# Kernel optimization log

Measured on AMD Instinct MI355X. Metric: run time of the kernel, lower is better.

## Reference

```python
import jax, jax.numpy as jnp
import numpy as np

N, B, S, F_DIM, E = 100000, 4096, 32, 256, 256


def _linear_params(key, fan_in, fan_out):
    kw, kb = jax.random.split(key)
    bound = 1.0 / np.sqrt(fan_in)
    W = jax.random.uniform(kw, (fan_in, fan_out), jnp.float32, -bound, bound)
    b = jax.random.uniform(kb, (fan_out,), jnp.float32, -bound, bound)
    return W, b


def setup_inputs() -> dict:
    key = jax.random.key(0)
    ks = jax.random.split(key, 10)
    Wm, bm = _linear_params(ks[4], F_DIM, E)
    Wq, bq = _linear_params(ks[5], F_DIM, E)
    Wk, bk = _linear_params(ks[6], F_DIM, E)
    Wv, bv = _linear_params(ks[7], F_DIM, E)
    Wc, bc = _linear_params(ks[8], 2 * E, E)
    return {
        "nodes": jax.random.randint(ks[0], (B,), 0, N),
        "neigh_mean": jax.random.randint(ks[1], (B, S), 0, N),
        "neigh_attn": jax.random.randint(ks[2], (B, S), 0, N),
        "id2feat": jax.random.normal(ks[3], (N, F_DIM), jnp.float32),
        "Wm": Wm, "bm": bm,
        "Wq": Wq, "bq": bq,
        "Wk": Wk, "bk": bk,
        "Wv": Wv, "bv": bv,
        "Wc": Wc, "bc": bc,
    }


def reference(nodes, neigh_mean, neigh_attn, id2feat,
              Wm, bm, Wq, bq, Wk, bk, Wv, bv, Wc, bc):
    self_feats = id2feat[nodes]                                   # [B, F]

    # MeanAggregator1: per-row mean of W(id2feat[neighbors]).
    # (mean(W x + b) == W mean(x) + b by linearity; all rows have S neighbors)
    ctx = jnp.mean(id2feat[neigh_mean], axis=1) @ Wm + bm          # [B, E]

    # AttnAggregator1: self-query attention over [neighbors ; self].
    neigh = id2feat[neigh_attn]                                    # [B, S, F]
    cat = jnp.concatenate([neigh, self_feats[:, None, :]], axis=1)  # [B, S+1, F]
    Q = self_feats @ Wq + bq                                       # [B, E]
    K = cat @ Wk + bk                                              # [B, S+1, E]
    V = cat @ Wv + bv                                              # [B, S+1, E]
    scores = jnp.einsum('be,bse->bs', Q, K)                        # [B, S+1]
    # Torch mask loop with uniform neighbor length S masks column S (the self slot)
    pad_mask = jnp.arange(S + 1) >= S                              # [S+1]
    scores = jnp.where(pad_mask[None, :], -jnp.inf, scores)
    attn = jax.nn.softmax(scores, axis=-1)
    mix = jnp.einsum('bs,bse->be', attn, V)                        # [B, E]

    combined = jnp.tanh(jnp.concatenate([mix, ctx], axis=-1) @ Wc + bc)  # [B, E]
    norm = jnp.linalg.norm(combined, axis=-1, keepdims=True)
    return combined / jnp.maximum(norm, 1e-12)                     # F.normalize(p=2)
```

## Files before the change

kernel.cpp:

```cpp
#include <hip/hip_runtime.h>
#include <math.h>

#define S_NEI 32

__global__ __launch_bounds__(256) void transpose256(const float* __restrict__ in,
                                                    float* __restrict__ outT) {
    __shared__ float tile[32][33];
    const int bx = blockIdx.x * 32, by = blockIdx.y * 32;
    const int x = threadIdx.x, y = threadIdx.y;
#pragma unroll
    for (int i = 0; i < 32; i += 8)
        tile[y + i][x] = in[(by + y + i) * 256 + bx + x];
    __syncthreads();
#pragma unroll
    for (int i = 0; i < 32; i += 8)
        outT[(bx + y + i) * 256 + by + x] = tile[x][y + i];
}

template <int KT>
__device__ __forceinline__ void gemm_tile8(const float* __restrict__ A, int row0,
                                           const float* __restrict__ B,
                                           float acc[2][4], float* __restrict__ sA,
                                           float* __restrict__ sB) {
    const int t = threadIdx.x;
    const int tr = t >> 6, tc = t & 63;
    const int r = t >> 5;
    const int k1 = t & 31;
    const size_t arow = (size_t)(row0 + r) * KT;
    for (int kb = 0; kb < KT; kb += 32) {
        sA[k1 * 12 + r] = A[arow + kb + k1];
#pragma unroll
        for (int i = 0; i < 8; ++i) {
            *reinterpret_cast<float4*>(&sB[(i * 4 + tr) * 256 + tc * 4]) =
                *reinterpret_cast<const float4*>(&B[(size_t)(kb + i * 4 + tr) * 256 + tc * 4]);
        }
        __syncthreads();
#pragma unroll
        for (int k = 0; k < 32; ++k) {
            const float2 a2 = *reinterpret_cast<const float2*>(&sA[k * 12 + tr * 2]);
            const float4 b4 = *reinterpret_cast<const float4*>(&sB[k * 256 + tc * 4]);
            acc[0][0] += a2.x * b4.x; acc[0][1] += a2.x * b4.y;
            acc[0][2] += a2.x * b4.z; acc[0][3] += a2.x * b4.w;
            acc[1][0] += a2.y * b4.x; acc[1][1] += a2.y * b4.y;
            acc[1][2] += a2.y * b4.z; acc[1][3] += a2.y * b4.w;
        }
        __syncthreads();
    }
}

__global__ __launch_bounds__(256) void precompute3(const float* __restrict__ Wq,
                                                   const float* __restrict__ Wv,
                                                   const float* __restrict__ Wm,
                                                   const float* __restrict__ Wc,
                                                   const float* __restrict__ WkT,
                                                   float* __restrict__ Wqk,
                                                   float* __restrict__ Wvc,
                                                   float* __restrict__ Wmc) {
    __shared__ float sA[32 * 12];
    __shared__ float sB[32 * 256];
    float acc[2][4] = {};
    const float *Ap, *Bp;
    float* Cp;
    switch (blockIdx.y) {
        case 0: Ap = Wq; Bp = WkT; Cp = Wqk; break;
        case 1: Ap = Wv; Bp = Wc; Cp = Wvc; break;
        default: Ap = Wm; Bp = Wc + 256 * 256; Cp = Wmc; break;
    }
    const int row0 = blockIdx.x * 8;
    gemm_tile8<256>(Ap, row0, Bp, acc, sA, sB);
    const int tr = threadIdx.x >> 6, tc = threadIdx.x & 63;
#pragma unroll
    for (int i = 0; i < 2; ++i) {
        float4 v = make_float4(acc[i][0], acc[i][1], acc[i][2], acc[i][3]);
        *reinterpret_cast<float4*>(&Cp[(row0 + tr * 2 + i) * 256 + tc * 4]) = v;
    }
}

__global__ __launch_bounds__(256) void bias_k(const float* __restrict__ bq,
                                              const float* __restrict__ bv,
                                              const float* __restrict__ bm,
                                              const float* __restrict__ bc,
                                              const float* __restrict__ Wc,
                                              const float* __restrict__ WkT,
                                              float* __restrict__ bqk,
                                              float* __restrict__ bfull) {
    const int c = blockIdx.x;
    const int e = threadIdx.x;
    const int w = e >> 6, l = e & 63;
    float a = bq[e] * WkT[e * 256 + c];
    float v = bv[e] * Wc[e * 256 + c] + bm[e] * Wc[(256 + e) * 256 + c];
    __shared__ float redA[4], redV[4];
#pragma unroll
    for (int off = 32; off; off >>= 1) { a += __shfl_xor(a, off); v += __shfl_xor(v, off); }
    if (l == 0) { redA[w] = a; redV[w] = v; }
    __syncthreads();
    if (e == 0) {
        bqk[c] = redA[0] + redA[1] + redA[2] + redA[3];
        bfull[c] = bc[c] + redV[0] + redV[1] + redV[2] + redV[3];
    }
}


#define SAF4(k) ((k) * 4 + ((((k) >> 3)) << 2))

#define FMA44(a4, b4)                                                       \
    do {                                                                    \
        acc[0][0] += (a4).x * (b4).x; acc[0][1] += (a4).x * (b4).y;         \
        acc[0][2] += (a4).x * (b4).z; acc[0][3] += (a4).x * (b4).w;         \
        acc[1][0] += (a4).y * (b4).x; acc[1][1] += (a4).y * (b4).y;         \
        acc[1][2] += (a4).y * (b4).z; acc[1][3] += (a4).y * (b4).w;         \
        acc[2][0] += (a4).z * (b4).x; acc[2][1] += (a4).z * (b4).y;         \
        acc[2][2] += (a4).z * (b4).z; acc[2][3] += (a4).z * (b4).w;         \
        acc[3][0] += (a4).w * (b4).x; acc[3][1] += (a4).w * (b4).y;         \
        acc[3][2] += (a4).w * (b4).z; acc[3][3] += (a4).w * (b4).w;         \
    } while (0)

__global__ __launch_bounds__(256, 2) void fused4(const float* __restrict__ id2feat,
                                                 const int* __restrict__ nodes,
                                                 const int* __restrict__ neigh_mean,
                                                 const int* __restrict__ neigh_attn,
                                                 const float* __restrict__ Wqk,
                                                 const float* __restrict__ bqk,
                                                 const float* __restrict__ Wfused,
                                                 const float* __restrict__ bfull,
                                                 float* __restrict__ out) {
    __shared__ __align__(16) char smem[18112];
    float* R0  = (float*)smem;
    float* sQk = (float*)(smem + 12480);
    int*   sIA = (int*)(smem + 16640);
    int*   sIM = (int*)(smem + 17152);

    const int t = threadIdx.x;
    const int w = t >> 6, l = t & 63;
    const int kq = w;
    const int col4 = l * 4;
    const int row0 = blockIdx.x * 4;

    if (t < 128) sIA[t] = neigh_attn[(size_t)row0 * S_NEI + t];
    else sIM[t - 128] = neigh_mean[(size_t)row0 * S_NEI + (t - 128)];

    {
        const float4 v = *reinterpret_cast<const float4*>(
            &id2feat[(size_t)nodes[row0 + w] * 256 + col4]);
        R0[SAF4(col4 + 0) + w] = v.x;
        R0[SAF4(col4 + 1) + w] = v.y;
        R0[SAF4(col4 + 2) + w] = v.z;
        R0[SAF4(col4 + 3) + w] = v.w;
    }
    __syncthreads();

    float acc[4][4] = {};

    {
        const float* Bp = Wqk + (size_t)(kq * 64) * 256 + col4;
        float4 bufA[8], bufB[8];
#pragma unroll
        for (int j = 0; j < 8; ++j)
            bufA[j] = *reinterpret_cast<const float4*>(&Bp[(size_t)j * 256]);
        for (int kb = 0; kb < 64; kb += 16) {
#pragma unroll
            for (int j = 0; j < 8; ++j)
                bufB[j] = *reinterpret_cast<const float4*>(&Bp[(size_t)(kb + 8 + j) * 256]);
#pragma unroll
            for (int j = 0; j < 8; ++j) {
                const float4 a4 = *reinterpret_cast<const float4*>(&R0[SAF4(kq * 64 + kb + j)]);
                FMA44(a4, bufA[j]);
            }
            if (kb + 16 < 64) {
#pragma unroll
                for (int j = 0; j < 8; ++j)
                    bufA[j] = *reinterpret_cast<const float4*>(&Bp[(size_t)(kb + 16 + j) * 256]);
            }
#pragma unroll
            for (int j = 0; j < 8; ++j) {
                const float4 a4 =
                    *reinterpret_cast<const float4*>(&R0[SAF4(kq * 64 + kb + 8 + j)]);
                FMA44(a4, bufB[j]);
            }
        }
    }
    __syncthreads();
    if (kq) {
        float* p = R0 + ((kq - 1) * 4) * 260 + col4;
#pragma unroll
        for (int r = 0; r < 4; ++r) {
            p[r * 260 + 0] = acc[r][0]; p[r * 260 + 1] = acc[r][1];
            p[r * 260 + 2] = acc[r][2]; p[r * 260 + 3] = acc[r][3];
        }
    }
    __syncthreads();
    if (kq == 0) {
        const float4 bq4 = *reinterpret_cast<const float4*>(&bqk[col4]);
#pragma unroll
        for (int r = 0; r < 4; ++r) {
            float v0 = acc[r][0] + bq4.x, v1 = acc[r][1] + bq4.y;
            float v2 = acc[r][2] + bq4.z, v3 = acc[r][3] + bq4.w;
#pragma unroll
            for (int s = 0; s < 3; ++s) {
                const float* p = R0 + (s * 4 + r) * 260 + col4;
                v0 += p[0]; v1 += p[1]; v2 += p[2]; v3 += p[3];
            }
            sQk[r * 260 + col4 + 0] = v0; sQk[r * 260 + col4 + 1] = v1;
            sQk[r * 260 + col4 + 2] = v2; sQk[r * 260 + col4 + 3] = v3;
        }
    }
    __syncthreads();

    {
        const int b = w;
        const float4 q = *reinterpret_cast<const float4*>(&sQk[b * 260 + col4]);
        const float4* f4 = reinterpret_cast<const float4*>(id2feat);
        const int* ia = sIA + b * 32;
        const int* im = sIM + b * 32;
        float4 macc = make_float4(0.f, 0.f, 0.f, 0.f);
        float4 wa = make_float4(0.f, 0.f, 0.f, 0.f);
        float m = -1e30f, e = 0.f;
#pragma unroll
        for (int cch = 0; cch < 4; ++cch) {
            float4 r[8];
#pragma unroll
            for (int j = 0; j < 8; ++j) r[j] = f4[(size_t)ia[cch * 8 + j] * 64 + l];
#pragma unroll
            for (int j = 0; j < 8; ++j) {
                const float4 v = f4[(size_t)im[cch * 8 + j] * 64 + l];
                macc.x += v.x; macc.y += v.y; macc.z += v.z; macc.w += v.w;
            }
            float p[8];
#pragma unroll
            for (int j = 0; j < 8; ++j) {
                float s = q.x * r[j].x + q.y * r[j].y + q.z * r[j].z + q.w * r[j].w;
#pragma unroll
                for (int off = 32; off; off >>= 1) s += __shfl_xor(s, off);
                p[j] = s;
            }
            float cm = p[0];
#pragma unroll
            for (int j = 1; j < 8; ++j) cm = fmaxf(cm, p[j]);
            const float newm = fmaxf(m, cm);
            const float sc = __expf(m - newm);
            e *= sc; wa.x *= sc; wa.y *= sc; wa.z *= sc; wa.w *= sc;
#pragma unroll
            for (int j = 0; j < 8; ++j) {
                const float g = __expf(p[j] - newm);
                e += g;
                wa.x += g * r[j].x; wa.y += g * r[j].y;
                wa.z += g * r[j].z; wa.w += g * r[j].w;
            }
            m = newm;
        }
        const float inv = 1.0f / e;
        const float mix[4] = {wa.x * inv, wa.y * inv, wa.z * inv, wa.w * inv};
        const float mev[4] = {macc.x * (1.f / 32), macc.y * (1.f / 32),
                              macc.z * (1.f / 32), macc.w * (1.f / 32)};
#pragma unroll
        for (int c = 0; c < 4; ++c) {
            R0[SAF4(col4 + c) + b] = mix[c];
            R0[SAF4(256 + col4 + c) + b] = mev[c];
        }
    }
    __syncthreads();

#pragma unroll
    for (int r = 0; r < 4; ++r)
#pragma unroll
        for (int c = 0; c < 4; ++c) acc[r][c] = 0.f;
    {
        const float* Bp = Wfused + (size_t)(kq * 128) * 256 + col4;
        float4 bufA[8], bufB[8];
#pragma unroll
        for (int j = 0; j < 8; ++j)
            bufA[j] = *reinterpret_cast<const float4*>(&Bp[(size_t)j * 256]);
        for (int kb = 0; kb < 128; kb += 16) {
#pragma unroll
            for (int j = 0; j < 8; ++j)
                bufB[j] = *reinterpret_cast<const float4*>(&Bp[(size_t)(kb + 8 + j) * 256]);
#pragma unroll
            for (int j = 0; j < 8; ++j) {
                const float4 a4 =
                    *reinterpret_cast<const float4*>(&R0[SAF4(kq * 128 + kb + j)]);
                FMA44(a4, bufA[j]);
            }
            if (kb + 16 < 128) {
#pragma unroll
                for (int j = 0; j < 8; ++j)
                    bufA[j] = *reinterpret_cast<const float4*>(&Bp[(size_t)(kb + 16 + j) * 256]);
            }
#pragma unroll
            for (int j = 0; j < 8; ++j) {
                const float4 a4 =
                    *reinterpret_cast<const float4*>(&R0[SAF4(kq * 128 + kb + 8 + j)]);
                FMA44(a4, bufB[j]);
            }
        }
    }
    __syncthreads();
    if (kq) {
        float* p = R0 + ((kq - 1) * 4) * 260 + col4;
#pragma unroll
        for (int r = 0; r < 4; ++r) {
            p[r * 260 + 0] = acc[r][0]; p[r * 260 + 1] = acc[r][1];
            p[r * 260 + 2] = acc[r][2]; p[r * 260 + 3] = acc[r][3];
        }
    }
    __syncthreads();
    if (kq == 0) {
        const float4 bf4 = *reinterpret_cast<const float4*>(&bfull[col4]);
#pragma unroll
        for (int r = 0; r < 4; ++r) {
            float v0 = acc[r][0] + bf4.x, v1 = acc[r][1] + bf4.y;
            float v2 = acc[r][2] + bf4.z, v3 = acc[r][3] + bf4.w;
#pragma unroll
            for (int s = 0; s < 3; ++s) {
                const float* p = R0 + (s * 4 + r) * 260 + col4;
                v0 += p[0]; v1 += p[1]; v2 += p[2]; v3 += p[3];
            }
            v0 = tanhf(v0); v1 = tanhf(v1); v2 = tanhf(v2); v3 = tanhf(v3);
            float sq = v0 * v0 + v1 * v1 + v2 * v2 + v3 * v3;
#pragma unroll
            for (int off = 32; off; off >>= 1) sq += __shfl_xor(sq, off);
            const float invn = 1.0f / fmaxf(sqrtf(sq), 1e-12f);
            *reinterpret_cast<float4*>(&out[(size_t)(row0 + r) * 256 + col4]) =
                make_float4(v0 * invn, v1 * invn, v2 * invn, v3 * invn);
        }
    }
}

extern "C" void kernel_launch(void* const* d_in, const int* in_sizes, int n_in,
                              void* d_out, int out_size, void* d_ws, size_t ws_size,
                              hipStream_t stream) {
    const int* nodes      = (const int*)d_in[0];
    const int* neigh_mean = (const int*)d_in[1];
    const int* neigh_attn = (const int*)d_in[2];
    const float* id2feat  = (const float*)d_in[3];
    const float* Wm = (const float*)d_in[4];
    const float* bm = (const float*)d_in[5];
    const float* Wq = (const float*)d_in[6];
    const float* bq = (const float*)d_in[7];
    const float* Wk = (const float*)d_in[8];
    const float* Wv = (const float*)d_in[10];
    const float* bv = (const float*)d_in[11];
    const float* Wc = (const float*)d_in[12];
    const float* bc = (const float*)d_in[13];
    float* out = (float*)d_out;

    const int B = in_sizes[0];

    float* ws    = (float*)d_ws;
    float* WkT   = ws;
    float* Wqk   = ws + 65536;
    float* Wvc   = ws + 131072;
    float* Wmc   = ws + 196608;
    float* bqk   = ws + 262144;
    float* bfull = ws + 262400;

    transpose256<<<dim3(8, 8), dim3(32, 8), 0, stream>>>(Wk, WkT);
    precompute3<<<dim3(32, 3), 256, 0, stream>>>(Wq, Wv, Wm, Wc, WkT, Wqk, Wvc, Wmc);
    bias_k<<<256, 256, 0, stream>>>(bq, bv, bm, bc, Wc, WkT, bqk, bfull);
    fused4<<<B / 4, 256, 0, stream>>>(id2feat, nodes, neigh_mean, neigh_attn,
                                      Wqk, bqk, Wvc , bfull, out);
}
```

Baseline: 88.75 us.

## Overlap neighbor gathers with Q GEMM and double-buffer attention gathers

Moves the mean-neighbor feature gathers into the Q projection GEMM loop so their global loads overlap with FMA work. The first attention-neighbor chunk is prefetched before the Q reduction barrier. Later chunks are double-buffered inside the online-softmax loop. The first Wfused weight tile is also loaded before the barrier. This hides gather latency behind compute at the cost of more live registers, which may reduce occupancy or cause spills.

```diff
diff --git a/kernel.cpp b/kernel.cpp
--- a/kernel.cpp
+++ b/kernel.cpp
@@ -149,36 +149,93 @@
     }
     __syncthreads();
 
+    const float4* f4 = reinterpret_cast<const float4*>(id2feat);
+    const int* im = sIM + w * 32;
+    const int* ia = sIA + w * 32;
+
     float acc[4][4] = {};
+    float4 macc = make_float4(0.f, 0.f, 0.f, 0.f);
 
     {
+        float4 mr0[4], mr1[4];
+#pragma unroll
+        for (int j = 0; j < 4; ++j) mr0[j] = f4[(size_t)im[j] * 64 + l];
+#pragma unroll
+        for (int j = 0; j < 4; ++j) mr1[j] = f4[(size_t)im[4 + j] * 64 + l];
+
         const float* Bp = Wqk + (size_t)(kq * 64) * 256 + col4;
-        float4 bufA[8], bufB[8];
-#pragma unroll
-        for (int j = 0; j < 8; ++j)
+        float4 bufA[4], bufB[4];
+#pragma unroll
+        for (int j = 0; j < 4; ++j)
             bufA[j] = *reinterpret_cast<const float4*>(&Bp[(size_t)j * 256]);
-        for (int kb = 0; kb < 64; kb += 16) {
-#pragma unroll
-            for (int j = 0; j < 8; ++j)
-                bufB[j] = *reinterpret_cast<const float4*>(&Bp[(size_t)(kb + 8 + j) * 256]);
-#pragma unroll
-            for (int j = 0; j < 8; ++j) {
-                const float4 a4 = *reinterpret_cast<const float4*>(&R0[SAF4(kq * 64 + kb + j)]);
+
+#pragma unroll
+        for (int ob = 0; ob < 4; ++ob) {
+            const int k0 = ob * 16;
+#pragma unroll
+            for (int j = 0; j < 4; ++j)
+                bufB[j] = *reinterpret_cast<const float4*>(&Bp[(size_t)(k0 + 4 + j) * 256]);
+#pragma unroll
+            for (int j = 0; j < 4; ++j) {
+                const float4 a4 = *reinterpret_cast<const float4*>(&R0[SAF4(kq * 64 + k0 + j)]);
                 FMA44(a4, bufA[j]);
             }
-            if (kb + 16 < 64) {
-#pragma unroll
-                for (int j = 0; j < 8; ++j)
-                    bufA[j] = *reinterpret_cast<const float4*>(&Bp[(size_t)(kb + 16 + j) * 256]);
-            }
-#pragma unroll
-            for (int j = 0; j < 8; ++j) {
+#pragma unroll
+            for (int j = 0; j < 4; ++j) {
+                macc.x += mr0[j].x; macc.y += mr0[j].y;
+                macc.z += mr0[j].z; macc.w += mr0[j].w;
+            }
+            if (ob < 3) {
+#pragma unroll
+                for (int j = 0; j < 4; ++j)
+                    mr0[j] = f4[(size_t)im[ob * 8 + 8 + j] * 64 + l];
+            }
+#pragma unroll
+            for (int j = 0; j < 4; ++j)
+                bufA[j] = *reinterpret_cast<const float4*>(&Bp[(size_t)(k0 + 8 + j) * 256]);
+#pragma unroll
+            for (int j = 0; j < 4; ++j) {
                 const float4 a4 =
-                    *reinterpret_cast<const float4*>(&R0[SAF4(kq * 64 + kb + 8 + j)]);
+                    *reinterpret_cast<const float4*>(&R0[SAF4(kq * 64 + k0 + 4 + j)]);
                 FMA44(a4, bufB[j]);
             }
-        }
-    }
+#pragma unroll
+            for (int j = 0; j < 4; ++j) {
+                macc.x += mr1[j].x; macc.y += mr1[j].y;
+                macc.z += mr1[j].z; macc.w += mr1[j].w;
+            }
+            if (ob < 3) {
+#pragma unroll
+                for (int j = 0; j < 4; ++j)
+                    mr1[j] = f4[(size_t)im[ob * 8 + 12 + j] * 64 + l];
+            }
+#pragma unroll
+            for (int j = 0; j < 4; ++j)
+                bufB[j] = *reinterpret_cast<const float4*>(&Bp[(size_t)(k0 + 12 + j) * 256]);
+#pragma unroll
+            for (int j = 0; j < 4; ++j) {
+                const float4 a4 =
+                    *reinterpret_cast<const float4*>(&R0[SAF4(kq * 64 + k0 + 8 + j)]);
+                FMA44(a4, bufA[j]);
+            }
+            if (ob < 3) {
+#pragma unroll
+                for (int j = 0; j < 4; ++j)
+                    bufA[j] = *reinterpret_cast<const float4*>(&Bp[(size_t)(k0 + 16 + j) * 256]);
+            }
+#pragma unroll
+            for (int j = 0; j < 4; ++j) {
+                const float4 a4 =
+                    *reinterpret_cast<const float4*>(&R0[SAF4(kq * 64 + k0 + 12 + j)]);
+                FMA44(a4, bufB[j]);
+            }
+        }
+    }
+
+    float4 rA[8], rB[8];
+#pragma unroll
+    for (int j = 0; j < 8; ++j) rA[j] = f4[(size_t)ia[j] * 64 + l];
+
     __syncthreads();
     if (kq) {
         float* p = R0 + ((kq - 1) * 4) * 260 + col4;
@@ -209,26 +266,21 @@
     {
         const int b = w;
         const float4 q = *reinterpret_cast<const float4*>(&sQk[b * 260 + col4]);
-        const float4* f4 = reinterpret_cast<const float4*>(id2feat);
-        const int* ia = sIA + b * 32;
-        const int* im = sIM + b * 32;
-        float4 macc = make_float4(0.f, 0.f, 0.f, 0.f);
+        float m = -1e30f, e = 0.f;
         float4 wa = make_float4(0.f, 0.f, 0.f, 0.f);
-        float m = -1e30f, e = 0.f;
-#pragma unroll
-        for (int cch = 0; cch < 4; ++cch) {
-            float4 r[8];
-#pragma unroll
-            for (int j = 0; j < 8; ++j) r[j] = f4[(size_t)ia[cch * 8 + j] * 64 + l];
+#pragma unroll
+        for (int c = 0; c < 4; ++c) {
+            const float4* rc = (c & 1) ? rB : rA;
+            float4* rn = (c & 1) ? rA : rB;
+            if (c < 3) {
+#pragma unroll
+                for (int j = 0; j < 8; ++j)
+                    rn[j] = f4[(size_t)ia[(c + 1) * 8 + j] * 64 + l];
+            }
+            float p[8];
 #pragma unroll
             for (int j = 0; j < 8; ++j) {
-                const float4 v = f4[(size_t)im[cch * 8 + j] * 64 + l];
-                macc.x += v.x; macc.y += v.y; macc.z += v.z; macc.w += v.w;
-            }
-            float p[8];
-#pragma unroll
-            for (int j = 0; j < 8; ++j) {
-                float s = q.x * r[j].x + q.y * r[j].y + q.z * r[j].z + q.w * r[j].w;
+                float s = q.x * rc[j].x + q.y * rc[j].y + q.z * rc[j].z + q.w * rc[j].w;
 #pragma unroll
                 for (int off = 32; off; off >>= 1) s += __shfl_xor(s, off);
                 p[j] = s;
@@ -243,54 +295,52 @@
             for (int j = 0; j < 8; ++j) {
                 const float g = __expf(p[j] - newm);
                 e += g;
-                wa.x += g * r[j].x; wa.y += g * r[j].y;
-                wa.z += g * r[j].z; wa.w += g * r[j].w;
+                wa.x += g * rc[j].x; wa.y += g * rc[j].y;
+                wa.z += g * rc[j].z; wa.w += g * rc[j].w;
             }
             m = newm;
         }
         const float inv = 1.0f / e;
-        const float mix[4] = {wa.x * inv, wa.y * inv, wa.z * inv, wa.w * inv};
+        const float mixv[4] = {wa.x * inv, wa.y * inv, wa.z * inv, wa.w * inv};
         const float mev[4] = {macc.x * (1.f / 32), macc.y * (1.f / 32),
                               macc.z * (1.f / 32), macc.w * (1.f / 32)};
 #pragma unroll
         for (int c = 0; c < 4; ++c) {
-            R0[SAF4(col4 + c) + b] = mix[c];
-            R0[SAF4(256 + col4 + c) + b] = mev[c];
-        }
-    }
+            R0[SAF4(col4 + c) + w] = mixv[c];
+            R0[SAF4(256 + col4 + c) + w] = mev[c];
+        }
+    }
+
+    const float* Bp3 = Wfused + (size_t)(kq * 128) * 256 + col4;
+    float4 bufA[8], bufB[8];
+#pragma unroll
+    for (int j = 0; j < 8; ++j)
+        bufA[j] = *reinterpret_cast<const float4*>(&Bp3[(size_t)j * 256]);
     __syncthreads();
 
 #pragma unroll
     for (int r = 0; r < 4; ++r)
 #pragma unroll
         for (int c = 0; c < 4; ++c) acc[r][c] = 0.f;
-    {
-        const float* Bp = Wfused + (size_t)(kq * 128) * 256 + col4;
-        float4 bufA[8], bufB[8];
+    for (int kb = 0; kb < 128; kb += 16) {
 #pragma unroll
         for (int j = 0; j < 8; ++j)
-            bufA[j] = *reinterpret_cast<const float4*>(&Bp[(size_t)j * 256]);
-        for (int kb = 0; kb < 128; kb += 16) {
+            bufB[j] = *reinterpret_cast<const float4*>(&Bp3[(size_t)(kb + 8 + j) * 256]);
+#pragma unroll
+        for (int j = 0; j < 8; ++j) {
+            const float4 a4 = *reinterpret_cast<const float4*>(&R0[SAF4(kq * 128 + kb + j)]);
+            FMA44(a4, bufA[j]);
+        }
+        if (kb + 16 < 128) {
 #pragma unroll
             for (int j = 0; j < 8; ++j)
-                bufB[j] = *reinterpret_cast<const float4*>(&Bp[(size_t)(kb + 8 + j) * 256]);
-#pragma unroll
-            for (int j = 0; j < 8; ++j) {
-                const float4 a4 =
-                    *reinterpret_cast<const float4*>(&R0[SAF4(kq * 128 + kb + j)]);
-                FMA44(a4, bufA[j]);
-            }
-            if (kb + 16 < 128) {
-#pragma unroll
-                for (int j = 0; j < 8; ++j)
-                    bufA[j] = *reinterpret_cast<const float4*>(&Bp[(size_t)(kb + 16 + j) * 256]);
-            }
-#pragma unroll
-            for (int j = 0; j < 8; ++j) {
-                const float4 a4 =
-                    *reinterpret_cast<const float4*>(&R0[SAF4(kq * 128 + kb + 8 + j)]);
-                FMA44(a4, bufB[j]);
-            }
+                bufA[j] = *reinterpret_cast<const float4*>(&Bp3[(size_t)(kb + 16 + j) * 256]);
+        }
+#pragma unroll
+        for (int j = 0; j < 8; ++j) {
+            const float4 a4 =
+                *reinterpret_cast<const float4*>(&R0[SAF4(kq * 128 + kb + 8 + j)]);
+            FMA44(a4, bufB[j]);
         }
     }
     __syncthreads();
```

Result: no change. 89.94 us (+1.3%).
